# Optimization experiments

Measured on AMD Instinct MI355X. Metric: run time of the kernel, lower is better.

The kernel has to match this reference:

```python
import jax, jax.numpy as jnp
import numpy as np

STATE_DIM = 1024
INPUT_DIM = 1024
OUTPUT_DIM = 1024
BATCH = 8
SEQ = 2048


def setup_inputs() -> dict:
    key = jax.random.key(0)
    k_x, k_a, k_b, k_w, k_bias = jax.random.split(key, 5)
    x = jax.random.normal(k_x, (BATCH, SEQ, INPUT_DIM), dtype=jnp.float32)
    # diagonal transition a in (0, 0.99) for stability
    A = jax.random.uniform(k_a, (STATE_DIM,), dtype=jnp.float32, minval=0.0, maxval=0.99)
    B = jax.random.normal(k_b, (STATE_DIM, INPUT_DIM), dtype=jnp.float32) / np.sqrt(INPUT_DIM)
    W = jax.random.normal(k_w, (OUTPUT_DIM, STATE_DIM), dtype=jnp.float32) / np.sqrt(STATE_DIM)
    b = jax.random.normal(k_bias, (OUTPUT_DIM,), dtype=jnp.float32) * 0.01
    return {"x": x, "A": A, "B": B, "W": W, "b": b}


def reference(x, A, B, W, b):
    # x: [batch, seq, input_dim]
    # Input projection: u_t = B x_t  -> [batch, seq, state_dim]
    u = jnp.einsum('bld,nd->bln', x, B)
    # Diagonal linear recurrence h_t = A * h_{t-1} + u_t via associative scan.
    # Pair representation (a, b) composes as (a1*a2, a2*b1 + b2).
    aa = jnp.broadcast_to(A, u.shape)

    def combine(c1, c2):
        a1, b1 = c1
        a2, b2 = c2
        return a1 * a2, a2 * b1 + b2

    _, h = jax.lax.associative_scan(combine, (aa, u), axis=1)
    # Output projection: [batch, seq, output_dim]
    return jnp.einsum('bln,on->blo', h, W) + b
```

## Files before the change

kernel.cpp:

```cpp
#include <hip/hip_runtime.h>
#include <stdint.h>

#define BATCH 8
#define SEQ 2048
#define DIM 1024
#define MTOT (BATCH * SEQ)

typedef __attribute__((ext_vector_type(8))) short short8;
typedef __attribute__((ext_vector_type(8))) unsigned short ushort8;
typedef __attribute__((ext_vector_type(4))) float floatx4;


__device__ __forceinline__ unsigned short f2bf(float f) {
  union { float f; unsigned u; } c; c.f = f;
  unsigned u = c.u;
  return (unsigned short)((u + 0x7FFFu + ((u >> 16) & 1u)) >> 16);
}
__device__ __forceinline__ float bf2f(unsigned short h) {
  union { unsigned u; float f; } c; c.u = ((unsigned)h) << 16;
  return c.f;
}

__device__ __forceinline__ void gll16(const void* g, void* l) {
  __builtin_amdgcn_global_load_lds(
      (__attribute__((address_space(1))) void*)(uintptr_t)g,
      (__attribute__((address_space(3))) void*)(uintptr_t)l,
      16, 0, 0);
}


#define X4 (MTOT * DIM / 4)
#define M4 (DIM * DIM / 4)

__global__ __launch_bounds__(256) void cast3_kernel(
    const float* __restrict__ x, const float* __restrict__ B,
    const float* __restrict__ W, unsigned short* __restrict__ xb,
    unsigned short* __restrict__ Bb, unsigned short* __restrict__ Wb) {
  int i = blockIdx.x * 256 + threadIdx.x;
  const float4* s4;
  uint2* d2;
  int li;
  if (i < X4) {
    s4 = (const float4*)x; d2 = (uint2*)xb; li = i;
  } else if (i < X4 + M4) {
    s4 = (const float4*)B; d2 = (uint2*)Bb; li = i - X4;
  } else {
    s4 = (const float4*)W; d2 = (uint2*)Wb; li = i - X4 - M4;
  }
  float4 v = s4[li];
  uint2 o;
  o.x = (unsigned)f2bf(v.x) | ((unsigned)f2bf(v.y) << 16);
  o.y = (unsigned)f2bf(v.z) | ((unsigned)f2bf(v.w) << 16);
  d2[li] = o;
}


__global__ __launch_bounds__(256) void gemm1_fused(
    const unsigned short* __restrict__ A,
    const unsigned short* __restrict__ B,
    unsigned short* __restrict__ u,
    const float* __restrict__ Adiag,
    float* __restrict__ aggbuf) {
  __shared__ unsigned short smem[16384];
  __shared__ float segsum[2][128];
  unsigned short* sA = smem;
  unsigned short* sB = smem + 8192;

  const int tid = threadIdx.x;
  const int wave = tid >> 6, lane = tid & 63;

  const int id = blockIdx.x;
  const int xcd = id & 7, j = id >> 3;
  const int mt = xcd * 16 + (j >> 3);
  const int nt = j & 7;
  const size_t m0 = (size_t)mt * 128;
  const int n0 = nt * 128;

  floatx4 acc[4][4] = {};

  const int srow = wave * 8 + (lane >> 3);
  const int scol = (((lane & 7) ^ ((lane >> 3) & 7)) * 8);
  const unsigned short* gA = A + (m0 + srow) * 1024 + scol;
  const unsigned short* gB = B + ((size_t)n0 + srow) * 1024 + scol;
  unsigned short* lA = sA + wave * 8 * 64;
  unsigned short* lB = sB + wave * 8 * 64;

  const int fr = lane & 15;
  const int frs = fr & 7;
  const int kb = lane >> 4;
  const int wm = (wave & 1) * 64, wn = (wave >> 1) * 64;

  for (int kt = 0; kt < 1024; kt += 64) {
#pragma unroll
    for (int r = 0; r < 4; ++r) {
      gll16(gA + (size_t)r * 32 * 1024 + kt, lA + r * 32 * 64);
      gll16(gB + (size_t)r * 32 * 1024 + kt, lB + r * 32 * 64);
    }
    asm volatile("s_waitcnt vmcnt(0)" ::: "memory");
    __syncthreads();
#pragma unroll
    for (int kk = 0; kk < 64; kk += 32) {
      short8 af[4], bfv[4];
#pragma unroll
      for (int i = 0; i < 4; ++i)
        af[i] = *(const short8*)(sA + (wm + i * 16 + fr) * 64 +
                                 ((((kk >> 3) + kb) ^ frs) * 8));
#pragma unroll
      for (int jj = 0; jj < 4; ++jj)
        bfv[jj] = *(const short8*)(sB + (wn + jj * 16 + fr) * 64 +
                                   ((((kk >> 3) + kb) ^ frs) * 8));
#pragma unroll
      for (int i = 0; i < 4; ++i)
#pragma unroll
        for (int jj = 0; jj < 4; ++jj)
          acc[i][jj] = __builtin_amdgcn_mfma_f32_16x16x32_bf16(
              af[i], bfv[jj], acc[i][jj], 0, 0, 0);
    }
    __syncthreads();
  }

  const int col = lane & 15;
  const int row4 = (lane >> 4) * 4;
  unsigned short* sC = smem;
#pragma unroll
  for (int i = 0; i < 4; ++i)
#pragma unroll
    for (int jj = 0; jj < 4; ++jj)
#pragma unroll
      for (int r = 0; r < 4; ++r)
        sC[(wm + i * 16 + row4 + r) * 128 + wn + jj * 16 + col] =
            f2bf(acc[i][jj][r]);
  __syncthreads();

  const int colv = tid & 127;
  const int seg = tid >> 7;
  const float a = Adiag[n0 + colv];
  {
    float s = 0.f;
    const int t0 = seg * 64;
#pragma unroll 8
    for (int t = 0; t < 64; ++t) {
      int idx = (t0 + t) * 128 + colv;
      s = fmaf(a, s, bf2f(sC[idx]));
      sC[idx] = f2bf(s);
    }
    segsum[seg][colv] = s;
  }
  __syncthreads();

  {
    float a2 = a * a, a4 = a2 * a2, a8 = a4 * a4, a16 = a8 * a8;
    float a32 = a16 * a16, a64 = a32 * a32;
    const float s0 = segsum[0][colv];
    const int t0 = 64 + seg * 32;
    float apow = seg ? a32 * a : a;
#pragma unroll 8
    for (int t = 0; t < 32; ++t) {
      int idx = (t0 + t) * 128 + colv;
      sC[idx] = f2bf(fmaf(apow, s0, bf2f(sC[idx])));
      apow *= a;
    }
    if (seg)
      aggbuf[(size_t)mt * 1024 + n0 + colv] =
          fmaf(a64, s0, segsum[1][colv]);
  }
  __syncthreads();

#pragma unroll
  for (int s = 0; s < 8; ++s) {
    int row = wave * 32 + s * 4 + (lane >> 4);
    int c8 = (lane & 15) * 8;
    *(ushort8*)(u + (m0 + row) * (size_t)1024 + n0 + c8) =
        *(const ushort8*)(sC + row * 128 + c8);
  }
}


__global__ __launch_bounds__(256) void apply_combined(
    unsigned short* __restrict__ u, const float* __restrict__ Adiag,
    const float* __restrict__ agg) {
  const int id = blockIdx.x;
  const int xcd = id & 7, rem = id >> 3;
  const int mt = xcd * 16 + (rem >> 4);
  const int sub = rem & 15;
  const int tg = threadIdx.x >> 7;
  const int ch0 = (threadIdx.x & 127) * 8;

  float a[8];
  *(float4*)&a[0] = *(const float4*)(Adiag + ch0);
  *(float4*)&a[4] = *(const float4*)(Adiag + ch0 + 4);

  float cf[8];
  {
    const int b = mt >> 4, c = mt & 15;
    float aL[8];
#pragma unroll
    for (int jj = 0; jj < 8; ++jj) aL[jj] = a[jj];
#pragma unroll
    for (int i = 0; i < 7; ++i)
#pragma unroll
      for (int jj = 0; jj < 8; ++jj) aL[jj] *= aL[jj];
#pragma unroll
    for (int jj = 0; jj < 8; ++jj) cf[jj] = 0.f;
    for (int cp = 0; cp < c; ++cp) {
      const float* ap = agg + (size_t)(b * 16 + cp) * 1024 + ch0;
      float lv[8];
      *(float4*)&lv[0] = *(const float4*)ap;
      *(float4*)&lv[4] = *(const float4*)(ap + 4);
#pragma unroll
      for (int jj = 0; jj < 8; ++jj) cf[jj] = fmaf(aL[jj], cf[jj], lv[jj]);
    }
  }

  const int tl = sub * 8 + tg * 4;
  float apow[8];
#pragma unroll
  for (int j = 0; j < 8; ++j)
    apow[j] = __builtin_amdgcn_exp2f(__builtin_amdgcn_logf(a[j]) *
                                     (float)(tl + 1));
  const size_t base = ((size_t)mt * 128 + tl) * DIM + ch0;
#pragma unroll
  for (int s = 0; s < 4; ++s) {
    ushort8 v = *(const ushort8*)(u + base + (size_t)s * DIM);
    ushort8 o;
#pragma unroll
    for (int j = 0; j < 8; ++j) {
      o[j] = f2bf(fmaf(apow[j], cf[j], bf2f(v[j])));
      apow[j] *= a[j];
    }
    *(ushort8*)(u + base + (size_t)s * DIM) = o;
  }
}


__global__ __launch_bounds__(512, 2) void gemm2_pipe(
    const unsigned short* __restrict__ A,
    const unsigned short* __restrict__ Bw,
    float* __restrict__ C, const float* __restrict__ bias) {
  extern __shared__ unsigned short sm[];

  const int tid = threadIdx.x;
  const int wid = tid >> 6, lane = tid & 63;

  const int id = blockIdx.x;
  const int xcd = id & 7, j = id >> 3;
  const int mt = xcd * 8 + (j >> 3);
  const int nt = j & 7;
  const size_t m0 = (size_t)mt * 256;
  const int n0 = nt * 128;

  floatx4 acc[4][4] = {};

  const int srow = tid >> 3;
  const int scolg = (tid & 7) ^ (srow & 7);
  const unsigned short* gA = A + (m0 + srow) * 1024 + scolg * 8;
  const unsigned short* gB = Bw + ((size_t)n0 + srow) * 1024 + scolg * 8;

  const int fr = lane & 15;
  const int frs = fr & 7;
  const int kb = lane >> 4;
  const int wm = (wid >> 1) * 64;
  const int wn = (wid & 1) * 64;

#define G2_STAGE(tt, s)                                                     \
  {                                                                         \
    const int kt_ = (tt) * 64;                                              \
    unsigned short* a_ = sm + (s) * 16384 + wid * 512;                      \
    unsigned short* b_ = sm + 49152 + (s) * 8192 + wid * 512;               \
    _Pragma("unroll") for (int r = 0; r < 4; ++r)                           \
        gll16(gA + (size_t)r * 64 * 1024 + kt_, a_ + r * 4096);             \
    _Pragma("unroll") for (int r = 0; r < 2; ++r)                           \
        gll16(gB + (size_t)r * 64 * 1024 + kt_, b_ + r * 4096);             \
  }

  G2_STAGE(0, 0);
  G2_STAGE(1, 1);
  asm volatile("s_waitcnt vmcnt(6)" ::: "memory");
  __syncthreads();

  for (int t = 0; t < 16; ++t) {
    if (t + 2 < 16) G2_STAGE(t + 2, (t + 2) % 3);

    const unsigned short* sA = sm + (t % 3) * 16384;
    const unsigned short* sB = sm + 49152 + (t % 3) * 8192;
    short8 af[4][2], bfv[4][2];
#pragma unroll
    for (int kk = 0; kk < 2; ++kk) {
#pragma unroll
      for (int i = 0; i < 4; ++i)
        af[i][kk] = *(const short8*)(sA + (wm + i * 16 + fr) * 64 +
                                     (((kk * 4 + kb) ^ frs) * 8));
#pragma unroll
      for (int jj = 0; jj < 4; ++jj)
        bfv[jj][kk] = *(const short8*)(sB + (wn + jj * 16 + fr) * 64 +
                                       (((kk * 4 + kb) ^ frs) * 8));
    }
    __builtin_amdgcn_s_setprio(1);
#pragma unroll
    for (int kk = 0; kk < 2; ++kk)
#pragma unroll
      for (int i = 0; i < 4; ++i)
#pragma unroll
        for (int jj = 0; jj < 4; ++jj)
          acc[i][jj] = __builtin_amdgcn_mfma_f32_16x16x32_bf16(
              af[i][kk], bfv[jj][kk], acc[i][jj], 0, 0, 0);
    __builtin_amdgcn_s_setprio(0);

    if (t + 2 < 16)
      asm volatile("s_waitcnt vmcnt(6)" ::: "memory");
    else
      asm volatile("s_waitcnt vmcnt(0)" ::: "memory");
    __syncthreads();
  }
#undef G2_STAGE

  const int col = lane & 15;
  const int row4 = (lane >> 4) * 4;
#pragma unroll
  for (int i = 0; i < 4; ++i)
#pragma unroll
    for (int jj = 0; jj < 4; ++jj)
#pragma unroll
      for (int r = 0; r < 4; ++r) {
        size_t m = m0 + wm + i * 16 + row4 + r;
        int n = n0 + wn + jj * 16 + col;
        C[m * 1024 + n] = acc[i][jj][r] + bias[n];
      }
}


extern "C" void kernel_launch(void* const* d_in, const int* in_sizes, int n_in,
                              void* d_out, int out_size, void* d_ws,
                              size_t ws_size, hipStream_t stream) {
  const float* x    = (const float*)d_in[0];
  const float* A    = (const float*)d_in[1];
  const float* B    = (const float*)d_in[2];
  const float* W    = (const float*)d_in[3];
  const float* bias = (const float*)d_in[4];

  char* ws = (char*)d_ws;
  unsigned short* xb   = (unsigned short*)ws;
  unsigned short* ubuf = (unsigned short*)(ws + 33554432);
  unsigned short* Bb   = (unsigned short*)(ws + 67108864);
  unsigned short* Wb   = (unsigned short*)(ws + 69206016);
  float* aggbuf        = (float*)(ws + 71303168);

  static bool attr_set = false;
  if (!attr_set) {
    hipFuncSetAttribute(reinterpret_cast<const void*>(gemm2_pipe),
                        hipFuncAttributeMaxDynamicSharedMemorySize, 147456);
    attr_set = true;
  }

  cast3_kernel<<<(X4 + 2 * M4) / 256, 256, 0, stream>>>(x, B, W, xb, Bb, Wb);

  gemm1_fused<<<1024, 256, 0, stream>>>(xb, Bb, ubuf, A, aggbuf);

  apply_combined<<<2048, 256, 0, stream>>>(ubuf, A, aggbuf);

  gemm2_pipe<<<512, 512, 147456, stream>>>(ubuf, Wb, (float*)d_out, bias);
}
```

Baseline: 230.9 us.

## Triple-buffer gemm1 K-loop with prefetch and skip first-chunk fixup

Measured after the change: 228.8 us. No clear change (-0.9%).

```diff
diff --git a/kernel.cpp b/kernel.cpp
--- a/kernel.cpp
+++ b/kernel.cpp
@@ -55,16 +55,14 @@
 }
 
 
-__global__ __launch_bounds__(256) void gemm1_fused(
+__global__ __launch_bounds__(256) void gemm1_r3(
     const unsigned short* __restrict__ A,
     const unsigned short* __restrict__ B,
     unsigned short* __restrict__ u,
     const float* __restrict__ Adiag,
     float* __restrict__ aggbuf) {
-  __shared__ unsigned short smem[16384];
+  __shared__ unsigned short smem[24576];
   __shared__ float segsum[2][128];
-  unsigned short* sA = smem;
-  unsigned short* sB = smem + 8192;
 
   const int tid = threadIdx.x;
   const int wave = tid >> 6, lane = tid & 63;
@@ -78,46 +76,63 @@
 
   floatx4 acc[4][4] = {};
 
-  const int srow = wave * 8 + (lane >> 3);
-  const int scol = (((lane & 7) ^ ((lane >> 3) & 7)) * 8);
-  const unsigned short* gA = A + (m0 + srow) * 1024 + scol;
-  const unsigned short* gB = B + ((size_t)n0 + srow) * 1024 + scol;
-  unsigned short* lA = sA + wave * 8 * 64;
-  unsigned short* lB = sB + wave * 8 * 64;
+  const int srow0 = wave * 16 + ((tid & 63) >> 2);
+  const int colg = (tid & 3) ^ ((tid >> 2) & 3);
+  const unsigned short* gA = A + (m0 + srow0) * 1024 + colg * 8;
+  const unsigned short* gB = B + ((size_t)n0 + srow0) * 1024 + colg * 8;
+  const int wofs = wave * 512;
 
   const int fr = lane & 15;
-  const int frs = fr & 7;
+  const int fm3 = fr & 3;
   const int kb = lane >> 4;
   const int wm = (wave & 1) * 64, wn = (wave >> 1) * 64;
 
-  for (int kt = 0; kt < 1024; kt += 64) {
-#pragma unroll
-    for (int r = 0; r < 4; ++r) {
-      gll16(gA + (size_t)r * 32 * 1024 + kt, lA + r * 32 * 64);
-      gll16(gB + (size_t)r * 32 * 1024 + kt, lB + r * 32 * 64);
-    }
-    asm volatile("s_waitcnt vmcnt(0)" ::: "memory");
+#define STG(tt, s)                                                          \
+  {                                                                         \
+    const int kt_ = (tt) * 32;                                              \
+    unsigned short* a_ = smem + (s) * 4096 + wofs;                          \
+    unsigned short* b_ = smem + 12288 + (s) * 4096 + wofs;                  \
+    gll16(gA + kt_, a_);                                                    \
+    gll16(gA + (size_t)64 * 1024 + kt_, a_ + 2048);                         \
+    gll16(gB + kt_, b_);                                                    \
+    gll16(gB + (size_t)64 * 1024 + kt_, b_ + 2048);                         \
+  }
+
+  STG(0, 0);
+  STG(1, 1);
+  asm volatile("s_waitcnt vmcnt(4)" ::: "memory");
+  __syncthreads();
+
+  for (int t = 0; t < 32; ++t) {
+    if (t + 2 < 32) STG(t + 2, (t + 2) % 3);
+
+    const unsigned short* sA = smem + (t % 3) * 4096;
+    const unsigned short* sB = smem + 12288 + (t % 3) * 4096;
+    short8 af[4], bfv[4];
+#pragma unroll
+    for (int i = 0; i < 4; ++i)
+      af[i] = *(const short8*)(sA + (wm + i * 16 + fr) * 32 +
+                               ((kb ^ fm3) * 8));
+#pragma unroll
+    for (int jj = 0; jj < 4; ++jj)
+      bfv[jj] = *(const short8*)(sB + (wn + jj * 16 + fr) * 32 +
+                                 ((kb ^ fm3) * 8));
+    __builtin_amdgcn_s_setprio(1);
+#pragma unroll
+    for (int i = 0; i < 4; ++i)
+#pragma unroll
+      for (int jj = 0; jj < 4; ++jj)
+        acc[i][jj] = __builtin_amdgcn_mfma_f32_16x16x32_bf16(
+            af[i], bfv[jj], acc[i][jj], 0, 0, 0);
+    __builtin_amdgcn_s_setprio(0);
+
+    if (t + 2 < 32)
+      asm volatile("s_waitcnt vmcnt(4)" ::: "memory");
+    else
+      asm volatile("s_waitcnt vmcnt(0)" ::: "memory");
     __syncthreads();
-#pragma unroll
-    for (int kk = 0; kk < 64; kk += 32) {
-      short8 af[4], bfv[4];
-#pragma unroll
-      for (int i = 0; i < 4; ++i)
-        af[i] = *(const short8*)(sA + (wm + i * 16 + fr) * 64 +
-                                 ((((kk >> 3) + kb) ^ frs) * 8));
-#pragma unroll
-      for (int jj = 0; jj < 4; ++jj)
-        bfv[jj] = *(const short8*)(sB + (wn + jj * 16 + fr) * 64 +
-                                   ((((kk >> 3) + kb) ^ frs) * 8));
-#pragma unroll
-      for (int i = 0; i < 4; ++i)
-#pragma unroll
-        for (int jj = 0; jj < 4; ++jj)
-          acc[i][jj] = __builtin_amdgcn_mfma_f32_16x16x32_bf16(
-              af[i], bfv[jj], acc[i][jj], 0, 0, 0);
-    }
-    __syncthreads();
-  }
+  }
+#undef STG
 
   const int col = lane & 15;
   const int row4 = (lane >> 4) * 4;
@@ -182,6 +197,7 @@
   const int id = blockIdx.x;
   const int xcd = id & 7, rem = id >> 3;
   const int mt = xcd * 16 + (rem >> 4);
+  if ((mt & 15) == 0) return;
   const int sub = rem & 15;
   const int tg = threadIdx.x >> 7;
   const int ch0 = (threadIdx.x & 127) * 8;
@@ -354,7 +370,7 @@
 
   cast3_kernel<<<(X4 + 2 * M4) / 256, 256, 0, stream>>>(x, B, W, xb, Bb, Wb);
 
-  gemm1_fused<<<1024, 256, 0, stream>>>(xb, Bb, ubuf, A, aggbuf);
+  gemm1_r3<<<1024, 256, 0, stream>>>(xb, Bb, ubuf, A, aggbuf);
 
   apply_combined<<<2048, 256, 0, stream>>>(ubuf, A, aggbuf);
 
```
